# Kernel optimization log

Hardware: AMD Instinct MI355X
Metric: run time of the kernel (lower is better)

## Reference

```python
import jax, jax.numpy as jnp
import numpy as np

NUM_HEADS = 16
CLAMP = 1e4


def setup_inputs() -> dict:
    key = jax.random.key(0)
    ks = jax.random.split(key, 8)
    B, Nq, Nkv, Cq, Ckv = 4, 2048, 2048, 1024, 768
    s_q = 1.0 / np.sqrt(Cq)
    s_kv = 1.0 / np.sqrt(Ckv)
    return {
        "query": jax.random.normal(ks[0], (B, Nq, Cq), jnp.float32),
        "key_value": jax.random.normal(ks[1], (B, Nkv, Ckv), jnp.float32),
        "Wq": jax.random.normal(ks[2], (Cq, Cq), jnp.float32) * s_q,
        "bq": jnp.zeros((Cq,), jnp.float32),
        "Wk": jax.random.normal(ks[3], (Ckv, Cq), jnp.float32) * s_kv,
        "bk": jnp.zeros((Cq,), jnp.float32),
        "Wv": jax.random.normal(ks[4], (Ckv, Cq), jnp.float32) * s_kv,
        "bv": jnp.zeros((Cq,), jnp.float32),
        "Wo": jax.random.normal(ks[5], (Cq, Cq), jnp.float32) * s_q,
        "bo": jnp.zeros((Cq,), jnp.float32),
    }


def reference(query, key_value, Wq, bq, Wk, bk, Wv, bv, Wo, bo):
    B, Nq, Cq = query.shape
    Nkv = key_value.shape[1]
    H = NUM_HEADS
    D = Cq // H
    scale = D ** (-0.5)

    # projections -> [B, H, N, D]
    q = (query @ Wq + bq).reshape(B, Nq, H, D).transpose(0, 2, 1, 3)
    k = (key_value @ Wk + bk).reshape(B, Nkv, H, D).transpose(0, 2, 1, 3)
    v = (key_value @ Wv + bv).reshape(B, Nkv, H, D).transpose(0, 2, 1, 3)

    # scores [B, H, Nq, Nkv] with clamp (mask=None path)
    attn = jnp.einsum("bhqd,bhkd->bhqk", q, k) * scale
    attn = jnp.clip(attn, -CLAMP, CLAMP)
    attn = jax.nn.softmax(attn, axis=-1)
    # NaN fallback: replace with uniform attention if any NaN present
    attn = jnp.where(jnp.any(jnp.isnan(attn)),
                     jnp.asarray(1.0 / Nkv, attn.dtype), attn)

    # weighted sum -> [B, Nq, Cq]
    x = jnp.einsum("bhqk,bhkd->bqhd", attn, v).reshape(B, Nq, Cq)
    return x @ Wo + bo
```

## Files before the change

kernel.cpp:

```cpp
#include <hip/hip_runtime.h>
#include <hip/hip_bf16.h>
#include <stdint.h>


typedef unsigned short u16;
typedef __attribute__((ext_vector_type(2))) float f32x2;
typedef __attribute__((ext_vector_type(4))) short bf16x4;
typedef __attribute__((ext_vector_type(8))) short bf16x8;
typedef __attribute__((ext_vector_type(4))) float f32x4;
typedef __attribute__((ext_vector_type(16))) float f32x16;

__device__ __forceinline__ u16 f2bf(float x) {
  union { float f; uint32_t u; } c; c.f = x;
  uint32_t r = c.u + 0x7fffu + ((c.u >> 16) & 1u);
  return (u16)(r >> 16);
}

__device__ __forceinline__ uint32_t pkbf(float a, float b) {
#if __has_builtin(__builtin_amdgcn_cvt_pk_bf16_f32)
  typedef __attribute__((ext_vector_type(2))) __bf16 bf2;
  bf2 r = __builtin_amdgcn_cvt_pk_bf16_f32(a, b);
  return __builtin_bit_cast(uint32_t, r);
#else
  return (uint32_t)f2bf(a) | ((uint32_t)f2bf(b) << 16);
#endif
}

__device__ __forceinline__ void gld16(const void* g, void* l) {
  __builtin_amdgcn_global_load_lds(
      (const __attribute__((address_space(1))) void*)g,
      (__attribute__((address_space(3))) void*)l, 16, 0, 0);
}

__device__ __forceinline__ void cvt_body(const float* __restrict__ in,
                                         u16* __restrict__ out, int blk) {
  int i = (blk * 256 + threadIdx.x) * 8;
  float4 a = *(const float4*)(in + i);
  float4 b = *(const float4*)(in + i + 4);
  union { u16 u[8]; uint4 v; } o;
  o.u[0] = f2bf(a.x); o.u[1] = f2bf(a.y); o.u[2] = f2bf(a.z); o.u[3] = f2bf(a.w);
  o.u[4] = f2bf(b.x); o.u[5] = f2bf(b.y); o.u[6] = f2bf(b.z); o.u[7] = f2bf(b.w);
  *(uint4*)(out + i) = o.v;
}

__device__ __forceinline__ void transpose_body(const float* __restrict__ in,
                                               u16* __restrict__ out,
                                               int R, int C, int bx, int by) {
  __shared__ float tile[64][65];
  int c0 = bx * 64, r0 = by * 64;
  #pragma unroll
  for (int it = 0; it < 16; it++) {
    int idx = threadIdx.x + it * 256;
    int lr = idx >> 6, lc = idx & 63;
    tile[lr][lc] = in[(size_t)(r0 + lr) * C + c0 + lc];
  }
  __syncthreads();
  #pragma unroll
  for (int it = 0; it < 16; it++) {
    int idx = threadIdx.x + it * 256;
    int lc = idx >> 6, lr = idx & 63;
    out[(size_t)(c0 + lc) * R + r0 + lr] = f2bf(tile[lr][lc]);
  }
}

__global__ void prep_kernel(const float* __restrict__ query,
                            const float* __restrict__ key_value,
                            const float* __restrict__ Wq, const float* __restrict__ Wk,
                            const float* __restrict__ Wv, const float* __restrict__ Wo,
                            u16* qb, u16* kvb, u16* WqT, u16* WkT, u16* WvT, u16* WoT) {
  int blk = blockIdx.x;
  if (blk < 4096) { cvt_body(query, qb, blk); return; }
  if (blk < 7168) { cvt_body(key_value, kvb, blk - 4096); return; }
  if (blk < 7424) { int lo = blk - 7168; transpose_body(Wq, WqT, 1024, 1024, lo & 15, lo >> 4); return; }
  if (blk < 7616) { int lo = blk - 7424; transpose_body(Wk, WkT, 768, 1024, lo & 15, lo >> 4); return; }
  if (blk < 7808) { int lo = blk - 7616; transpose_body(Wv, WvT, 768, 1024, lo & 15, lo >> 4); return; }
  { int lo = blk - 7808; transpose_body(Wo, WoT, 1024, 1024, lo & 15, lo >> 4); return; }
}

template<bool SWAP>
__device__ __forceinline__ void gemm_kloop(const u16* __restrict__ A,
                                           const u16* __restrict__ BT,
                                           int K, char* smem, f32x4 (&acc)[4][4],
                                           int m0, int n0, int tid) {
  const u16* ap[4]; const u16* bp[4]; int ldA[4], ldB[4];
  #pragma unroll
  for (int it2 = 0; it2 < 4; it2++) {
    int s = it2 * 256 + tid;
    int row = s >> 3, cl = (s & 7) ^ (row & 7);
    ap[it2] = A + (size_t)(m0 + row) * K + cl * 8;
    bp[it2] = BT + (size_t)(n0 + row) * K + cl * 8;
    ldA[it2] = s * 16;
    ldB[it2] = 16384 + s * 16;
  }
  const int w = tid >> 6, l = tid & 63;
  const int lm = l & 15, lq = l >> 4;
  const int wr = w >> 1, wc = w & 1;
  int abase[4], bbase[4];
  #pragma unroll
  for (int i = 0; i < 4; i++) {
    int m = wr * 64 + i * 16 + lm;
    abase[i] = m * 128 + ((lq ^ (m & 7)) << 4);
    int n = wc * 64 + i * 16 + lm;
    bbase[i] = 16384 + n * 128 + ((lq ^ (n & 7)) << 4);
  }
  for (int k0 = 0; k0 < K; k0 += 64) {
    #pragma unroll
    for (int it2 = 0; it2 < 4; it2++) {
      gld16(ap[it2], smem + ldA[it2]);
      gld16(bp[it2], smem + ldB[it2]);
      ap[it2] += 64; bp[it2] += 64;
    }
    __syncthreads();
    #pragma unroll
    for (int kk = 0; kk < 2; kk++) {
      bf16x8 af[4], bf[4];
      #pragma unroll
      for (int i = 0; i < 4; i++)
        af[i] = *(const bf16x8*)(smem + (abase[i] ^ (kk << 6)));
      #pragma unroll
      for (int j = 0; j < 4; j++)
        bf[j] = *(const bf16x8*)(smem + (bbase[j] ^ (kk << 6)));
      #pragma unroll
      for (int i = 0; i < 4; i++)
        #pragma unroll
        for (int j = 0; j < 4; j++) {
          if (SWAP)
            acc[i][j] = __builtin_amdgcn_mfma_f32_16x16x32_bf16(bf[j], af[i], acc[i][j], 0, 0, 0);
          else
            acc[i][j] = __builtin_amdgcn_mfma_f32_16x16x32_bf16(af[i], bf[j], acc[i][j], 0, 0, 0);
        }
    }
    __syncthreads();
  }
}

__global__ __launch_bounds__(256, 4)
void gemm_qkv(const u16* __restrict__ qb, const u16* __restrict__ kvb,
              const u16* __restrict__ WqT, const u16* __restrict__ WkT,
              const u16* __restrict__ WvT,
              const float* __restrict__ bq, const float* __restrict__ bk,
              const float* __restrict__ bv,
              u16* __restrict__ Qb, u16* __restrict__ Kbf, u16* __restrict__ Vt,
              float qscale) {
  extern __shared__ __align__(16) char smem[];
  const int tid = threadIdx.x;
  const int w = tid >> 6, l = tid & 63;
  const int lm = l & 15, lq = l >> 4;
  const int m0 = blockIdx.y * 128, n0 = blockIdx.x * 128;
  const int wr = w >> 1, wc = w & 1;
  const int z = blockIdx.z;
  f32x4 acc[4][4] = {};

  u16* etile = (u16*)(smem + w * 9216);
  const int xr = l >> 3, cc = (l & 7) ^ xr;

  if (z < 2) {
    const u16* A = (z == 0) ? qb : kvb;
    const u16* BT = (z == 0) ? WqT : WkT;
    const float* bias = (z == 0) ? bq : bk;
    u16* out = (z == 0) ? Qb : Kbf;
    const float scale = (z == 0) ? qscale : 1.0f;
    const int K = (z == 0) ? 1024 : 768;
    gemm_kloop<true>(A, BT, K, smem, acc, m0, n0, tid);
    #pragma unroll
    for (int j = 0; j < 4; j++) {
      float4 b4 = *(const float4*)&bias[n0 + wc * 64 + j * 16 + lq * 4];
      #pragma unroll
      for (int i = 0; i < 4; i++) {
        uint2 pkd;
        pkd.x = pkbf((acc[i][j][0] + b4.x) * scale, (acc[i][j][1] + b4.y) * scale);
        pkd.y = pkbf((acc[i][j][2] + b4.z) * scale, (acc[i][j][3] + b4.w) * scale);
        *(uint2*)&etile[(i * 16 + lm) * 72 + j * 16 + lq * 4] = pkd;
      }
    }
    u16* gbase = out + (size_t)(m0 + wr * 64) * 1024 + n0 + wc * 64;
    #pragma unroll
    for (int co = 0; co < 8; co++) {
      int ml = co * 8 + xr;
      uint4 d = *(const uint4*)&etile[ml * 72 + cc * 8];
      *(uint4*)&gbase[(size_t)ml * 1024 + cc * 8] = d;
    }
  } else {
    gemm_kloop<false>(kvb, WvT, 768, smem, acc, m0, n0, tid);
    #pragma unroll
    for (int j = 0; j < 4; j++) {
      float bi = bv[n0 + wc * 64 + j * 16 + lm];
      #pragma unroll
      for (int i = 0; i < 4; i++) {
        uint2 pkd;
        pkd.x = pkbf(acc[i][j][0] + bi, acc[i][j][1] + bi);
        pkd.y = pkbf(acc[i][j][2] + bi, acc[i][j][3] + bi);
        *(uint2*)&etile[(j * 16 + lm) * 72 + i * 16 + lq * 4] = pkd;
      }
    }
    const int bb = m0 >> 11, mloc = (m0 & 2047) + wr * 64;
    u16* gbase = Vt + ((size_t)bb * 1024 + n0 + wc * 64) * 2048 + mloc;
    const int kvA = (cc >> 1) * 16 + (cc & 1) * 4;
    #pragma unroll
    for (int co = 0; co < 8; co++) {
      int dl = co * 8 + xr;
      uint2 dA = *(const uint2*)&etile[dl * 72 + kvA];
      uint2 dB = *(const uint2*)&etile[dl * 72 + kvA + 8];
      uint4 d = {dA.x, dA.y, dB.x, dB.y};
      *(uint4*)&gbase[(size_t)dl * 2048 + cc * 8] = d;
    }
  }
}

__global__ __launch_bounds__(256, 4)
void gemm_o(const u16* __restrict__ A, const u16* __restrict__ BT,
            const float* __restrict__ bias, float* __restrict__ Cout) {
  __shared__ __align__(16) char smem[32768];
  const int tid = threadIdx.x;
  const int w = tid >> 6, l = tid & 63;
  const int lm = l & 15, lq = l >> 4;
  const int m0 = blockIdx.y * 128, n0 = blockIdx.x * 128;
  const int wr = w >> 1, wc = w & 1;
  f32x4 acc[4][4] = {};
  gemm_kloop<false>(A, BT, 1024, smem, acc, m0, n0, tid);
  #pragma unroll
  for (int j = 0; j < 4; j++) {
    int gn = n0 + wc * 64 + j * 16 + lm;
    float bi = bias[gn];
    #pragma unroll
    for (int i = 0; i < 4; i++) {
      int gm = m0 + wr * 64 + i * 16 + lq * 4;
      #pragma unroll
      for (int r = 0; r < 4; r++)
        Cout[(size_t)(gm + r) * 1024 + gn] = acc[i][j][r] + bi;
    }
  }
}

__global__ __launch_bounds__(256, 2)
void attn_kernel(const u16* __restrict__ Q, const u16* __restrict__ Kb,
                 const u16* __restrict__ Vt, u16* __restrict__ X) {
  __shared__ __align__(16) char smem[32768];
  const int tid = threadIdx.x, w = tid >> 6, l = tid & 63;
  const int l31 = l & 31, h5 = l >> 5;
  const int bh = blockIdx.x, b = bh >> 4, h = bh & 15;
  const int q0 = blockIdx.y * 256 + w * 64;
  const int rx = l31 & 7;

  const u16* Kg = Kb + (size_t)b * 2048 * 1024 + h * 64;
  const u16* Vg = Vt + (size_t)bh * 64 * 2048;

  const u16 *kp0, *kp1, *vp0, *vp1;
  {
    int s = tid, r = s >> 3, c = (s & 7) ^ (r & 7);
    kp0 = Kg + (size_t)r * 1024 + c * 8;
    vp0 = Vg + (size_t)r * 2048 + c * 8;
    s = 256 + tid; r = s >> 3; c = (s & 7) ^ (r & 7);
    kp1 = Kg + (size_t)r * 1024 + c * 8;
    vp1 = Vg + (size_t)r * 2048 + c * 8;
  }
  const int kd0 = tid * 16, kd1 = (256 + tid) * 16;

  bf16x8 qfA[4], qfB[4];
  {
    const u16* qp = Q + ((size_t)(b * 2048 + q0 + l31)) * 1024 + h * 64 + h5 * 8;
    #pragma unroll
    for (int t = 0; t < 4; t++) qfA[t] = *(const bf16x8*)(qp + t * 16);
    qp += (size_t)32 * 1024;
    #pragma unroll
    for (int t = 0; t < 4; t++) qfB[t] = *(const bf16x8*)(qp + t * 16);
  }

  const int kvb2 = (l31 << 7) | ((rx ^ h5) << 4);
  const int vb2 = 16384 | (l31 << 7) | ((rx ^ h5) << 4);

  f32x16 xaccA[2] = {}, xaccB[2] = {};
  f32x2 lsA = {0.f, 0.f}, lsB = {0.f, 0.f};
  const f32x16 KZ = {};

  gld16(kp0, smem + kd0); gld16(kp1, smem + kd1);
  gld16(vp0, smem + 16384 + kd0); gld16(vp1, smem + 16384 + kd1);
  kp0 += 65536; kp1 += 65536; vp0 += 64; vp1 += 64;
  __syncthreads();

#define ATTN_STEP(CUR, DOPREF)                                                  \
  {                                                                             \
    if (DOPREF) {                                                               \
      const int nb = ((CUR) ^ 1) << 13;                                         \
      gld16(kp0, smem + nb + kd0); gld16(kp1, smem + nb + kd1);                 \
      gld16(vp0, smem + 16384 + nb + kd0); gld16(vp1, smem + 16384 + nb + kd1); \
      kp0 += 65536; kp1 += 65536; vp0 += 64; vp1 += 64;                         \
    }                                                                           \
    _Pragma("unroll")                                                           \
    for (int sub = 0; sub < 2; sub++) {                                         \
      const int km = ((CUR) << 13) | (sub << 12);                               \
      bf16x8 kf[4];                                                             \
      _Pragma("unroll")                                                         \
      for (int t = 0; t < 4; t++)                                               \
        kf[t] = *(const bf16x8*)(smem + (kvb2 ^ (km | (t << 5))));              \
      f32x16 st = __builtin_amdgcn_mfma_f32_32x32x16_bf16(kf[0], qfA[0], KZ, 0, 0, 0); \
      _Pragma("unroll")                                                         \
      for (int t = 1; t < 4; t++)                                               \
        st = __builtin_amdgcn_mfma_f32_32x32x16_bf16(kf[t], qfA[t], st, 0, 0, 0); \
      uint32_t pkA[8], pkB[8];                                                  \
      _Pragma("unroll")                                                         \
      for (int u = 0; u < 4; u++) {                                             \
        float p0 = __builtin_amdgcn_exp2f(st[4 * u + 0]);                       \
        float p1 = __builtin_amdgcn_exp2f(st[4 * u + 1]);                       \
        float p2 = __builtin_amdgcn_exp2f(st[4 * u + 2]);                       \
        float p3 = __builtin_amdgcn_exp2f(st[4 * u + 3]);                       \
        lsA += (f32x2){p0 + p2, p1 + p3};                                       \
        pkA[2 * u] = pkbf(p0, p1); pkA[2 * u + 1] = pkbf(p2, p3);               \
      }                                                                         \
      st = __builtin_amdgcn_mfma_f32_32x32x16_bf16(kf[0], qfB[0], KZ, 0, 0, 0); \
      _Pragma("unroll")                                                         \
      for (int t = 1; t < 4; t++)                                               \
        st = __builtin_amdgcn_mfma_f32_32x32x16_bf16(kf[t], qfB[t], st, 0, 0, 0); \
      _Pragma("unroll")                                                         \
      for (int u = 0; u < 4; u++) {                                             \
        float p0 = __builtin_amdgcn_exp2f(st[4 * u + 0]);                       \
        float p1 = __builtin_amdgcn_exp2f(st[4 * u + 1]);                       \
        float p2 = __builtin_amdgcn_exp2f(st[4 * u + 2]);                       \
        float p3 = __builtin_amdgcn_exp2f(st[4 * u + 3]);                       \
        lsB += (f32x2){p0 + p2, p1 + p3};                                       \
        pkB[2 * u] = pkbf(p0, p1); pkB[2 * u + 1] = pkbf(p2, p3);               \
      }                                                                         \
      _Pragma("unroll")                                                         \
      for (int c2 = 0; c2 < 2; c2++) {                                          \
        union { uint32_t d[4]; bf16x8 v; } pfA, pfB;                            \
        _Pragma("unroll")                                                       \
        for (int dd = 0; dd < 4; dd++) {                                        \
          pfA.d[dd] = pkA[4 * c2 + dd]; pfB.d[dd] = pkB[4 * c2 + dd];           \
        }                                                                       \
        const int vx = ((sub << 2) | (c2 << 1)) << 4;                           \
        _Pragma("unroll")                                                       \
        for (int dt = 0; dt < 2; dt++) {                                        \
          bf16x8 vf = *(const bf16x8*)(smem +                                   \
              (vb2 ^ (((CUR) << 13) | (dt << 12) | vx)));                       \
          xaccA[dt] = __builtin_amdgcn_mfma_f32_32x32x16_bf16(vf, pfA.v, xaccA[dt], 0, 0, 0); \
          xaccB[dt] = __builtin_amdgcn_mfma_f32_32x32x16_bf16(vf, pfB.v, xaccB[dt], 0, 0, 0); \
        }                                                                       \
      }                                                                         \
    }                                                                           \
    __syncthreads();                                                            \
  }

  for (int itp = 0; itp < 15; itp++) {
    ATTN_STEP(0, true)
    ATTN_STEP(1, true)
  }
  ATTN_STEP(0, true)
  ATTN_STEP(1, false)
#undef ATTN_STEP

  {
    float lsum = lsA[0] + lsA[1];
    const float inv = 1.0f / (lsum + __shfl_xor(lsum, 32));
    u16* xp = X + ((size_t)(b * 2048 + q0 + l31)) * 1024 + h * 64;
    #pragma unroll
    for (int dt = 0; dt < 2; dt++)
      #pragma unroll
      for (int g = 0; g < 4; g++) {
        const int d0 = dt * 32 + g * 8 + h5 * 4;
        uint2 o;
        o.x = pkbf(xaccA[dt][4 * g + 0] * inv, xaccA[dt][4 * g + 1] * inv);
        o.y = pkbf(xaccA[dt][4 * g + 2] * inv, xaccA[dt][4 * g + 3] * inv);
        *(uint2*)(xp + d0) = o;
      }
  }
  {
    float lsum = lsB[0] + lsB[1];
    const float inv = 1.0f / (lsum + __shfl_xor(lsum, 32));
    u16* xp = X + ((size_t)(b * 2048 + q0 + 32 + l31)) * 1024 + h * 64;
    #pragma unroll
    for (int dt = 0; dt < 2; dt++)
      #pragma unroll
      for (int g = 0; g < 4; g++) {
        const int d0 = dt * 32 + g * 8 + h5 * 4;
        uint2 o;
        o.x = pkbf(xaccB[dt][4 * g + 0] * inv, xaccB[dt][4 * g + 1] * inv);
        o.y = pkbf(xaccB[dt][4 * g + 2] * inv, xaccB[dt][4 * g + 3] * inv);
        *(uint2*)(xp + d0) = o;
      }
  }
}

extern "C" void kernel_launch(void* const* d_in, const int* in_sizes, int n_in,
                              void* d_out, int out_size, void* d_ws, size_t ws_size,
                              hipStream_t stream) {
  const float* query     = (const float*)d_in[0];
  const float* key_value = (const float*)d_in[1];
  const float* Wq = (const float*)d_in[2];
  const float* bq = (const float*)d_in[3];
  const float* Wk = (const float*)d_in[4];
  const float* bk = (const float*)d_in[5];
  const float* Wv = (const float*)d_in[6];
  const float* bv = (const float*)d_in[7];
  const float* Wo = (const float*)d_in[8];
  const float* bo = (const float*)d_in[9];
  float* out = (float*)d_out;

  char* ws = (char*)d_ws;
  size_t off = 0;
  auto alloc = [&](size_t bytes) -> void* {
    void* p = ws + off; off += (bytes + 255) & ~(size_t)255; return p;
  };
  u16* qb  = (u16*)alloc((size_t)8192 * 1024 * 2);
  u16* kvb = (u16*)alloc((size_t)8192 * 768 * 2);
  u16* WqT = (u16*)alloc((size_t)1024 * 1024 * 2);
  u16* WkT = (u16*)alloc((size_t)1024 * 768 * 2);
  u16* WvT = (u16*)alloc((size_t)1024 * 768 * 2);
  u16* WoT = (u16*)alloc((size_t)1024 * 1024 * 2);
  u16* Qb  = (u16*)alloc((size_t)8192 * 1024 * 2);
  u16* Kbf = (u16*)alloc((size_t)8192 * 1024 * 2);
  u16* Vt  = (u16*)alloc((size_t)8192 * 1024 * 2);
  u16* Xb  = (u16*)alloc((size_t)8192 * 1024 * 2);

  prep_kernel<<<8064, 256, 0, stream>>>(query, key_value, Wq, Wk, Wv, Wo,
                                        qb, kvb, WqT, WkT, WvT, WoT);

  const float qscale = 0.125f * 1.4426950408889634f;
  gemm_qkv<<<dim3(8, 64, 3), 256, 36864, stream>>>(qb, kvb, WqT, WkT, WvT,
                                                   bq, bk, bv, Qb, Kbf, Vt, qscale);

  attn_kernel<<<dim3(64, 8), 256, 0, stream>>>(Qb, Kbf, Vt, Xb);

  gemm_o<<<dim3(8, 64), 256, 0, stream>>>(Xb, WoT, bo, out);
}
```

Baseline: 323.5 us.

## Triple-buffer GEMM k-loop with 256x128 tiles and 8-wave blocks

Replaces the single-buffered GEMM main loop with a three-stage LDS ring. Global-to-LDS loads for tile t+2 are issued while MFMAs run on tile t, using explicit vmcnt/lgkmcnt waits, raw barriers and setprio around the MFMA bursts. The QKV and output GEMMs switch to 512-thread blocks computing 256x128 output tiles, which halves the grid and increases B-operand reuse. In exchange, the 144KB static LDS allows only one block per CU, so latency hiding relies on the software pipeline rather than on occupancy.

```diff
diff --git a/kernel.cpp b/kernel.cpp
--- a/kernel.cpp
+++ b/kernel.cpp
@@ -78,19 +78,26 @@
 }
 
 template<bool SWAP>
-__device__ __forceinline__ void gemm_kloop(const u16* __restrict__ A,
-                                           const u16* __restrict__ BT,
-                                           int K, char* smem, f32x4 (&acc)[4][4],
-                                           int m0, int n0, int tid) {
-  const u16* ap[4]; const u16* bp[4]; int ldA[4], ldB[4];
-  #pragma unroll
-  for (int it2 = 0; it2 < 4; it2++) {
-    int s = it2 * 256 + tid;
+__device__ __forceinline__ void kloop3(const u16* __restrict__ A,
+                                       const u16* __restrict__ BT,
+                                       int K, char* smem, f32x4 (&acc)[4][4],
+                                       int m0, int n0, int tid) {
+  const int NT = K >> 6;
+  const u16* ap[4]; const u16* bp[2];
+  int adst[4], bdst[2];
+  #pragma unroll
+  for (int it = 0; it < 4; it++) {
+    int s = it * 512 + tid;
     int row = s >> 3, cl = (s & 7) ^ (row & 7);
-    ap[it2] = A + (size_t)(m0 + row) * K + cl * 8;
-    bp[it2] = BT + (size_t)(n0 + row) * K + cl * 8;
-    ldA[it2] = s * 16;
-    ldB[it2] = 16384 + s * 16;
+    ap[it] = A + (size_t)(m0 + row) * K + cl * 8;
+    adst[it] = s * 16;
+  }
+  #pragma unroll
+  for (int it = 0; it < 2; it++) {
+    int s = it * 512 + tid;
+    int row = s >> 3, cl = (s & 7) ^ (row & 7);
+    bp[it] = BT + (size_t)(n0 + row) * K + cl * 8;
+    bdst[it] = 32768 + s * 16;
   }
   const int w = tid >> 6, l = tid & 63;
   const int lm = l & 15, lq = l >> 4;
@@ -101,40 +108,97 @@
     int m = wr * 64 + i * 16 + lm;
     abase[i] = m * 128 + ((lq ^ (m & 7)) << 4);
     int n = wc * 64 + i * 16 + lm;
-    bbase[i] = 16384 + n * 128 + ((lq ^ (n & 7)) << 4);
-  }
-  for (int k0 = 0; k0 < K; k0 += 64) {
-    #pragma unroll
-    for (int it2 = 0; it2 < 4; it2++) {
-      gld16(ap[it2], smem + ldA[it2]);
-      gld16(bp[it2], smem + ldB[it2]);
-      ap[it2] += 64; bp[it2] += 64;
-    }
-    __syncthreads();
-    #pragma unroll
-    for (int kk = 0; kk < 2; kk++) {
-      bf16x8 af[4], bf[4];
-      #pragma unroll
-      for (int i = 0; i < 4; i++)
-        af[i] = *(const bf16x8*)(smem + (abase[i] ^ (kk << 6)));
-      #pragma unroll
-      for (int j = 0; j < 4; j++)
-        bf[j] = *(const bf16x8*)(smem + (bbase[j] ^ (kk << 6)));
-      #pragma unroll
-      for (int i = 0; i < 4; i++)
-        #pragma unroll
-        for (int j = 0; j < 4; j++) {
-          if (SWAP)
-            acc[i][j] = __builtin_amdgcn_mfma_f32_16x16x32_bf16(bf[j], af[i], acc[i][j], 0, 0, 0);
-          else
-            acc[i][j] = __builtin_amdgcn_mfma_f32_16x16x32_bf16(af[i], bf[j], acc[i][j], 0, 0, 0);
-        }
-    }
-    __syncthreads();
-  }
-}
-
-__global__ __launch_bounds__(256, 4)
+    bbase[i] = 32768 + n * 128 + ((lq ^ (n & 7)) << 4);
+  }
+  #pragma unroll
+  for (int it = 0; it < 4; it++) { gld16(ap[it], smem + adst[it]); ap[it] += 64; }
+  #pragma unroll
+  for (int it = 0; it < 2; it++) { gld16(bp[it], smem + bdst[it]); bp[it] += 64; }
+  #pragma unroll
+  for (int it = 0; it < 4; it++) { gld16(ap[it], smem + 49152 + adst[it]); ap[it] += 64; }
+  #pragma unroll
+  for (int it = 0; it < 2; it++) { gld16(bp[it], smem + 49152 + bdst[it]); bp[it] += 64; }
+  asm volatile("s_waitcnt vmcnt(6)" ::: "memory");
+  __builtin_amdgcn_s_barrier();
+  asm volatile("" ::: "memory");
+
+#define GMFMA16(XORK)                                                           \
+      _Pragma("unroll")                                                         \
+      for (int i = 0; i < 4; i++)                                               \
+        _Pragma("unroll")                                                       \
+        for (int j = 0; j < 4; j++)                                             \
+          acc[i][j] = SWAP                                                      \
+            ? __builtin_amdgcn_mfma_f32_16x16x32_bf16(bf[j], af[i], acc[i][j], 0, 0, 0) \
+            : __builtin_amdgcn_mfma_f32_16x16x32_bf16(af[i], bf[j], acc[i][j], 0, 0, 0);
+
+#define GTILE(T_, BI_)                                                          \
+  {                                                                             \
+    const int BB = (BI_) * 49152;                                               \
+    const int SB = (((BI_) + 2) % 3) * 49152;                                   \
+    const bool st = (T_) + 2 < NT;                                              \
+    {                                                           \
+      bf16x8 af[4], bf[4];                                                      \
+      _Pragma("unroll")                                                         \
+      for (int i = 0; i < 4; i++)                                               \
+        af[i] = *(const bf16x8*)(smem + BB + abase[i]);                         \
+      _Pragma("unroll")                                                         \
+      for (int j = 0; j < 4; j++)                                               \
+        bf[j] = *(const bf16x8*)(smem + BB + bbase[j]);                         \
+      if (st) {                                                                 \
+        gld16(ap[0], smem + SB + adst[0]);                                      \
+        gld16(ap[1], smem + SB + adst[1]);                                      \
+        gld16(bp[0], smem + SB + bdst[0]);                                      \
+      }                                                                         \
+      __builtin_amdgcn_s_barrier();                                             \
+      asm volatile("s_waitcnt lgkmcnt(0)" ::: "memory");                        \
+      __builtin_amdgcn_sched_barrier(0);                                        \
+      __builtin_amdgcn_s_setprio(1);                                            \
+      GMFMA16(0)                                                                \
+      __builtin_amdgcn_s_setprio(0);                                            \
+      __builtin_amdgcn_s_barrier();                                             \
+      asm volatile("" ::: "memory");                                            \
+    }                                                                           \
+    {                                                           \
+      bf16x8 af[4], bf[4];                                                      \
+      _Pragma("unroll")                                                         \
+      for (int i = 0; i < 4; i++)                                               \
+        af[i] = *(const bf16x8*)(smem + BB + (abase[i] ^ 64));                  \
+      _Pragma("unroll")                                                         \
+      for (int j = 0; j < 4; j++)                                               \
+        bf[j] = *(const bf16x8*)(smem + BB + (bbase[j] ^ 64));                  \
+      if (st) {                                                                 \
+        gld16(ap[2], smem + SB + adst[2]);                                      \
+        gld16(ap[3], smem + SB + adst[3]);                                      \
+        gld16(bp[1], smem + SB + bdst[1]);                                      \
+        ap[0] += 64; ap[1] += 64; ap[2] += 64; ap[3] += 64;                     \
+        bp[0] += 64; bp[1] += 64;                                               \
+      }                                                                         \
+      if ((T_) + 1 < NT) {                                                      \
+        if (st) asm volatile("s_waitcnt vmcnt(6)" ::: "memory");                \
+        else    asm volatile("s_waitcnt vmcnt(0)" ::: "memory");                \
+      }                                                                         \
+      __builtin_amdgcn_s_barrier();                                             \
+      asm volatile("s_waitcnt lgkmcnt(0)" ::: "memory");                        \
+      __builtin_amdgcn_sched_barrier(0);                                        \
+      __builtin_amdgcn_s_setprio(1);                                            \
+      GMFMA16(1)                                                                \
+      __builtin_amdgcn_s_setprio(0);                                            \
+      __builtin_amdgcn_s_barrier();                                             \
+      asm volatile("" ::: "memory");                                            \
+    }                                                                           \
+  }
+
+  for (int t = 0; t < NT; t += 3) {
+    GTILE(t, 0)
+    if (t + 1 < NT) GTILE(t + 1, 1)
+    if (t + 2 < NT) GTILE(t + 2, 2)
+  }
+#undef GTILE
+#undef GMFMA16
+  __syncthreads();
+}
+
+__global__ __launch_bounds__(512, 2)
 void gemm_qkv(const u16* __restrict__ qb, const u16* __restrict__ kvb,
               const u16* __restrict__ WqT, const u16* __restrict__ WkT,
               const u16* __restrict__ WvT,
@@ -142,11 +206,11 @@
               const float* __restrict__ bv,
               u16* __restrict__ Qb, u16* __restrict__ Kbf, u16* __restrict__ Vt,
               float qscale) {
-  extern __shared__ __align__(16) char smem[];
+  __shared__ __align__(16) char smem[147456];
   const int tid = threadIdx.x;
   const int w = tid >> 6, l = tid & 63;
   const int lm = l & 15, lq = l >> 4;
-  const int m0 = blockIdx.y * 128, n0 = blockIdx.x * 128;
+  const int m0 = blockIdx.y * 256, n0 = blockIdx.x * 128;
   const int wr = w >> 1, wc = w & 1;
   const int z = blockIdx.z;
   f32x4 acc[4][4] = {};
@@ -161,7 +225,7 @@
     u16* out = (z == 0) ? Qb : Kbf;
     const float scale = (z == 0) ? qscale : 1.0f;
     const int K = (z == 0) ? 1024 : 768;
-    gemm_kloop<true>(A, BT, K, smem, acc, m0, n0, tid);
+    kloop3<true>(A, BT, K, smem, acc, m0, n0, tid);
     #pragma unroll
     for (int j = 0; j < 4; j++) {
       float4 b4 = *(const float4*)&bias[n0 + wc * 64 + j * 16 + lq * 4];
@@ -181,7 +245,7 @@
       *(uint4*)&gbase[(size_t)ml * 1024 + cc * 8] = d;
     }
   } else {
-    gemm_kloop<false>(kvb, WvT, 768, smem, acc, m0, n0, tid);
+    kloop3<false>(kvb, WvT, 768, smem, acc, m0, n0, tid);
     #pragma unroll
     for (int j = 0; j < 4; j++) {
       float bi = bv[n0 + wc * 64 + j * 16 + lm];
@@ -207,17 +271,17 @@
   }
 }
 
-__global__ __launch_bounds__(256, 4)
+__global__ __launch_bounds__(512, 2)
 void gemm_o(const u16* __restrict__ A, const u16* __restrict__ BT,
             const float* __restrict__ bias, float* __restrict__ Cout) {
-  __shared__ __align__(16) char smem[32768];
+  __shared__ __align__(16) char smem[147456];
   const int tid = threadIdx.x;
   const int w = tid >> 6, l = tid & 63;
   const int lm = l & 15, lq = l >> 4;
-  const int m0 = blockIdx.y * 128, n0 = blockIdx.x * 128;
+  const int m0 = blockIdx.y * 256, n0 = blockIdx.x * 128;
   const int wr = w >> 1, wc = w & 1;
   f32x4 acc[4][4] = {};
-  gemm_kloop<false>(A, BT, 1024, smem, acc, m0, n0, tid);
+  kloop3<false>(A, BT, 1024, smem, acc, m0, n0, tid);
   #pragma unroll
   for (int j = 0; j < 4; j++) {
     int gn = n0 + wc * 64 + j * 16 + lm;
@@ -415,10 +479,10 @@
                                         qb, kvb, WqT, WkT, WvT, WoT);
 
   const float qscale = 0.125f * 1.4426950408889634f;
-  gemm_qkv<<<dim3(8, 64, 3), 256, 36864, stream>>>(qb, kvb, WqT, WkT, WvT,
-                                                   bq, bk, bv, Qb, Kbf, Vt, qscale);
+  gemm_qkv<<<dim3(8, 32, 3), 512, 0, stream>>>(qb, kvb, WqT, WkT, WvT,
+                                               bq, bk, bv, Qb, Kbf, Vt, qscale);
 
   attn_kernel<<<dim3(64, 8), 256, 0, stream>>>(Qb, Kbf, Vt, Xb);
 
-  gemm_o<<<dim3(8, 64), 256, 0, stream>>>(Xb, WoT, bo, out);
-}
+  gemm_o<<<dim3(8, 32), 512, 0, stream>>>(Xb, WoT, bo, out);
+}
```

Result: faster. 292.6 us (-9.5%).

## Enlarge GEMM tiles to 256x256 with 512 threads and double-buffered LDS

Applied to the files above, without the earlier changes.

Replaces the 128x128 GEMM k-loop used by the QKV and output projections with a 256x256 tile computed by 8 waves. Global-to-LDS loads for the next K slice now go into a second buffer while the current one is consumed, removing one barrier per iteration. The aim is more operand reuse per loaded byte and load/compute overlap. In exchange, each block uses about 128–144 KB of LDS, so only one block fits per CU. The grids also shrink to 384 and 128 blocks, which may leave CUs idle, especially for the output projection.

```diff
diff --git a/kernel.cpp b/kernel.cpp
--- a/kernel.cpp
+++ b/kernel.cpp
@@ -78,50 +78,66 @@
 }
 
 template<bool SWAP>
-__device__ __forceinline__ void gemm_kloop(const u16* __restrict__ A,
-                                           const u16* __restrict__ BT,
-                                           int K, char* smem, f32x4 (&acc)[4][4],
-                                           int m0, int n0, int tid) {
-  const u16* ap[4]; const u16* bp[4]; int ldA[4], ldB[4];
-  #pragma unroll
-  for (int it2 = 0; it2 < 4; it2++) {
-    int s = it2 * 256 + tid;
+__device__ __forceinline__ void kloop256(const u16* __restrict__ A,
+                                         const u16* __restrict__ BT,
+                                         int K, char* smem, f32x4 (&acc)[8][4],
+                                         int m0, int n0, int tid) {
+  const int NT = K >> 6;
+  const u16* ap[4]; const u16* bp[4];
+  int adst[4], bdst[4];
+  #pragma unroll
+  for (int it = 0; it < 4; it++) {
+    int s = it * 512 + tid;
     int row = s >> 3, cl = (s & 7) ^ (row & 7);
-    ap[it2] = A + (size_t)(m0 + row) * K + cl * 8;
-    bp[it2] = BT + (size_t)(n0 + row) * K + cl * 8;
-    ldA[it2] = s * 16;
-    ldB[it2] = 16384 + s * 16;
+    ap[it] = A + (size_t)(m0 + row) * K + cl * 8;
+    adst[it] = s * 16;
+    bp[it] = BT + (size_t)(n0 + row) * K + cl * 8;
+    bdst[it] = 32768 + s * 16;
   }
   const int w = tid >> 6, l = tid & 63;
   const int lm = l & 15, lq = l >> 4;
-  const int wr = w >> 1, wc = w & 1;
-  int abase[4], bbase[4];
-  #pragma unroll
-  for (int i = 0; i < 4; i++) {
-    int m = wr * 64 + i * 16 + lm;
+  const int wr = w >> 2, wc = w & 3;
+  int abase[8], bbase[4];
+  #pragma unroll
+  for (int i = 0; i < 8; i++) {
+    int m = wr * 128 + i * 16 + lm;
     abase[i] = m * 128 + ((lq ^ (m & 7)) << 4);
-    int n = wc * 64 + i * 16 + lm;
-    bbase[i] = 16384 + n * 128 + ((lq ^ (n & 7)) << 4);
-  }
-  for (int k0 = 0; k0 < K; k0 += 64) {
-    #pragma unroll
-    for (int it2 = 0; it2 < 4; it2++) {
-      gld16(ap[it2], smem + ldA[it2]);
-      gld16(bp[it2], smem + ldB[it2]);
-      ap[it2] += 64; bp[it2] += 64;
-    }
-    __syncthreads();
+  }
+  #pragma unroll
+  for (int j = 0; j < 4; j++) {
+    int n = wc * 64 + j * 16 + lm;
+    bbase[j] = 32768 + n * 128 + ((lq ^ (n & 7)) << 4);
+  }
+  #pragma unroll
+  for (int it = 0; it < 4; it++) gld16(ap[it], smem + adst[it]);
+  #pragma unroll
+  for (int it = 0; it < 4; it++) gld16(bp[it], smem + bdst[it]);
+  #pragma unroll
+  for (int it = 0; it < 4; it++) { ap[it] += 64; bp[it] += 64; }
+  __syncthreads();
+
+  for (int t = 0; t < NT; t++) {
+    const int BB = (t & 1) << 16;
+    if (t + 1 < NT) {
+      const int SB = BB ^ 65536;
+      #pragma unroll
+      for (int it = 0; it < 4; it++) gld16(ap[it], smem + SB + adst[it]);
+      #pragma unroll
+      for (int it = 0; it < 4; it++) gld16(bp[it], smem + SB + bdst[it]);
+      #pragma unroll
+      for (int it = 0; it < 4; it++) { ap[it] += 64; bp[it] += 64; }
+    }
     #pragma unroll
     for (int kk = 0; kk < 2; kk++) {
-      bf16x8 af[4], bf[4];
-      #pragma unroll
-      for (int i = 0; i < 4; i++)
-        af[i] = *(const bf16x8*)(smem + (abase[i] ^ (kk << 6)));
+      bf16x8 af[8], bf[4];
+      #pragma unroll
+      for (int i = 0; i < 8; i++)
+        af[i] = *(const bf16x8*)(smem + BB + (abase[i] ^ (kk << 6)));
       #pragma unroll
       for (int j = 0; j < 4; j++)
-        bf[j] = *(const bf16x8*)(smem + (bbase[j] ^ (kk << 6)));
-      #pragma unroll
-      for (int i = 0; i < 4; i++)
+        bf[j] = *(const bf16x8*)(smem + BB + (bbase[j] ^ (kk << 6)));
+      #pragma unroll
+      for (int i = 0; i < 8; i++)
         #pragma unroll
         for (int j = 0; j < 4; j++) {
           if (SWAP)
@@ -134,7 +150,7 @@
   }
 }
 
-__global__ __launch_bounds__(256, 4)
+__global__ __launch_bounds__(512, 2)
 void gemm_qkv(const u16* __restrict__ qb, const u16* __restrict__ kvb,
               const u16* __restrict__ WqT, const u16* __restrict__ WkT,
               const u16* __restrict__ WvT,
@@ -142,16 +158,16 @@
               const float* __restrict__ bv,
               u16* __restrict__ Qb, u16* __restrict__ Kbf, u16* __restrict__ Vt,
               float qscale) {
-  extern __shared__ __align__(16) char smem[];
+  __shared__ __align__(16) char smem[147456];
   const int tid = threadIdx.x;
   const int w = tid >> 6, l = tid & 63;
   const int lm = l & 15, lq = l >> 4;
-  const int m0 = blockIdx.y * 128, n0 = blockIdx.x * 128;
-  const int wr = w >> 1, wc = w & 1;
+  const int m0 = blockIdx.y * 256, n0 = blockIdx.x * 256;
+  const int wr = w >> 2, wc = w & 3;
   const int z = blockIdx.z;
-  f32x4 acc[4][4] = {};
-
-  u16* etile = (u16*)(smem + w * 9216);
+  f32x4 acc[8][4] = {};
+
+  u16* etile = (u16*)(smem + w * 18432);
   const int xr = l >> 3, cc = (l & 7) ^ xr;
 
   if (z < 2) {
@@ -161,70 +177,71 @@
     u16* out = (z == 0) ? Qb : Kbf;
     const float scale = (z == 0) ? qscale : 1.0f;
     const int K = (z == 0) ? 1024 : 768;
-    gemm_kloop<true>(A, BT, K, smem, acc, m0, n0, tid);
+    kloop256<true>(A, BT, K, smem, acc, m0, n0, tid);
     #pragma unroll
     for (int j = 0; j < 4; j++) {
       float4 b4 = *(const float4*)&bias[n0 + wc * 64 + j * 16 + lq * 4];
       #pragma unroll
-      for (int i = 0; i < 4; i++) {
+      for (int i = 0; i < 8; i++) {
         uint2 pkd;
         pkd.x = pkbf((acc[i][j][0] + b4.x) * scale, (acc[i][j][1] + b4.y) * scale);
         pkd.y = pkbf((acc[i][j][2] + b4.z) * scale, (acc[i][j][3] + b4.w) * scale);
         *(uint2*)&etile[(i * 16 + lm) * 72 + j * 16 + lq * 4] = pkd;
       }
     }
-    u16* gbase = out + (size_t)(m0 + wr * 64) * 1024 + n0 + wc * 64;
-    #pragma unroll
-    for (int co = 0; co < 8; co++) {
+    u16* gbase = out + (size_t)(m0 + wr * 128) * 1024 + n0 + wc * 64;
+    #pragma unroll
+    for (int co = 0; co < 16; co++) {
       int ml = co * 8 + xr;
       uint4 d = *(const uint4*)&etile[ml * 72 + cc * 8];
       *(uint4*)&gbase[(size_t)ml * 1024 + cc * 8] = d;
     }
   } else {
-    gemm_kloop<false>(kvb, WvT, 768, smem, acc, m0, n0, tid);
+    kloop256<false>(kvb, WvT, 768, smem, acc, m0, n0, tid);
     #pragma unroll
     for (int j = 0; j < 4; j++) {
       float bi = bv[n0 + wc * 64 + j * 16 + lm];
       #pragma unroll
-      for (int i = 0; i < 4; i++) {
+      for (int i = 0; i < 8; i++) {
         uint2 pkd;
         pkd.x = pkbf(acc[i][j][0] + bi, acc[i][j][1] + bi);
         pkd.y = pkbf(acc[i][j][2] + bi, acc[i][j][3] + bi);
-        *(uint2*)&etile[(j * 16 + lm) * 72 + i * 16 + lq * 4] = pkd;
+        *(uint2*)&etile[(j * 16 + lm) * 136 + i * 16 + lq * 4] = pkd;
       }
     }
-    const int bb = m0 >> 11, mloc = (m0 & 2047) + wr * 64;
+    const int bb = m0 >> 11, mloc = (m0 & 2047) + wr * 128;
     u16* gbase = Vt + ((size_t)bb * 1024 + n0 + wc * 64) * 2048 + mloc;
-    const int kvA = (cc >> 1) * 16 + (cc & 1) * 4;
-    #pragma unroll
-    for (int co = 0; co < 8; co++) {
-      int dl = co * 8 + xr;
-      uint2 dA = *(const uint2*)&etile[dl * 72 + kvA];
-      uint2 dB = *(const uint2*)&etile[dl * 72 + kvA + 8];
+    #pragma unroll
+    for (int co = 0; co < 16; co++) {
+      int dl = (co & 7) * 8 + xr;
+      int cx = (co >> 3) * 8 + cc;
+      const int kvA = (cx >> 1) * 16 + (cx & 1) * 4;
+      uint2 dA = *(const uint2*)&etile[dl * 136 + kvA];
+      uint2 dB = *(const uint2*)&etile[dl * 136 + kvA + 8];
       uint4 d = {dA.x, dA.y, dB.x, dB.y};
-      *(uint4*)&gbase[(size_t)dl * 2048 + cc * 8] = d;
-    }
-  }
-}
-
-__global__ __launch_bounds__(256, 4)
+      *(uint4*)&gbase[(size_t)dl * 2048 + cx * 8] = d;
+    }
+  }
+}
+
+__global__ __launch_bounds__(512, 2)
 void gemm_o(const u16* __restrict__ A, const u16* __restrict__ BT,
             const float* __restrict__ bias, float* __restrict__ Cout) {
-  __shared__ __align__(16) char smem[32768];
+  __shared__ __align__(16) char smem[131072];
   const int tid = threadIdx.x;
   const int w = tid >> 6, l = tid & 63;
   const int lm = l & 15, lq = l >> 4;
-  const int m0 = blockIdx.y * 128, n0 = blockIdx.x * 128;
-  const int wr = w >> 1, wc = w & 1;
-  f32x4 acc[4][4] = {};
-  gemm_kloop<false>(A, BT, 1024, smem, acc, m0, n0, tid);
+  const int m0 = blockIdx.y * 256, n0 = blockIdx.x * 256;
+  const int wr = w >> 2, wc = w & 3;
+  f32x4 acc[8][4] = {};
+  kloop256<false>(A, BT, 1024, smem, acc, m0, n0, tid);
   #pragma unroll
   for (int j = 0; j < 4; j++) {
     int gn = n0 + wc * 64 + j * 16 + lm;
     float bi = bias[gn];
     #pragma unroll
-    for (int i = 0; i < 4; i++) {
-      int gm = m0 + wr * 64 + i * 16 + lq * 4;
+    for (int i = 0; i < 8; i++) {
+      int gm = m0 + wr * 128 + i * 16 + lq * 4;
       #pragma unroll
       for (int r = 0; r < 4; r++)
         Cout[(size_t)(gm + r) * 1024 + gn] = acc[i][j][r] + bi;
@@ -415,10 +432,10 @@
                                         qb, kvb, WqT, WkT, WvT, WoT);
 
   const float qscale = 0.125f * 1.4426950408889634f;
-  gemm_qkv<<<dim3(8, 64, 3), 256, 36864, stream>>>(qb, kvb, WqT, WkT, WvT,
-                                                   bq, bk, bv, Qb, Kbf, Vt, qscale);
+  gemm_qkv<<<dim3(4, 32, 3), 512, 0, stream>>>(qb, kvb, WqT, WkT, WvT,
+                                               bq, bk, bv, Qb, Kbf, Vt, qscale);
 
   attn_kernel<<<dim3(64, 8), 256, 0, stream>>>(Qb, Kbf, Vt, Xb);
 
-  gemm_o<<<dim3(8, 64), 256, 0, stream>>>(Xb, WoT, bo, out);
-}
+  gemm_o<<<dim3(4, 32), 512, 0, stream>>>(Xb, WoT, bo, out);
+}
```

After: 295.4 us. 1.1x faster.
